# Kernel tuning notes

Hardware: AMD Instinct MI355X
Metric: run time of the kernel (lower is better)

## Reference

```python
import jax, jax.numpy as jnp
import numpy as np

N = 50000
E = 800000
IN_DIM = 128
HIDDEN = 256
HP = HIDDEN // 3            # 85
HP2 = HIDDEN - 2 * HP       # 86
OUT_DIM = 40


def setup_inputs() -> dict:
    key = jax.random.key(0)
    ks = jax.random.split(key, 10)
    x = jax.random.normal(ks[0], (N, IN_DIM), dtype=jnp.float32)
    edge_index = jax.random.randint(ks[1], (2, E), 0, N, dtype=jnp.int64)
    s = 1.0 / np.sqrt(IN_DIM)
    W0 = jax.random.uniform(ks[2], (IN_DIM, HP), jnp.float32, -s, s)
    b0 = jax.random.uniform(ks[3], (HP,), jnp.float32, -s, s)
    W1 = jax.random.uniform(ks[4], (IN_DIM, HP), jnp.float32, -s, s)
    b1 = jax.random.uniform(ks[5], (HP,), jnp.float32, -s, s)
    W2 = jax.random.uniform(ks[6], (IN_DIM, HP2), jnp.float32, -s, s)
    b2 = jax.random.uniform(ks[7], (HP2,), jnp.float32, -s, s)
    sf = 1.0 / np.sqrt(HIDDEN)
    Wf = jax.random.uniform(ks[8], (HIDDEN, OUT_DIM), jnp.float32, -sf, sf)
    bf = jax.random.uniform(ks[9], (OUT_DIM,), jnp.float32, -sf, sf)
    return {"x": x, "edge_index": edge_index, "W0": W0, "b0": b0,
            "W1": W1, "b1": b1, "W2": W2, "b2": b2, "Wf": Wf, "bf": bf}


def _spmm(row, col, x, n):
    # adj @ x where adj[row[e], col[e]] = 1 : gather neighbor feats, scatter-add to row
    return jax.ops.segment_sum(x[col], row, num_segments=n)


def reference(x, edge_index, W0, b0, W1, b1, W2, b2, Wf, bf):
    n = x.shape[0]
    row, col = edge_index[0], edge_index[1]
    # out-degree of row nodes, clamped to min 1
    deg = jax.ops.segment_sum(jnp.ones((row.shape[0],), x.dtype), row, num_segments=n)
    deg_inv = 1.0 / jnp.maximum(deg, 1.0)
    # hop 0
    h0 = x @ W0 + b0
    # hop 1: (A x) * deg_inv
    ax = _spmm(row, col, x, n)
    h1 = (ax * deg_inv[:, None]) @ W1 + b1
    # hop 2: (A A x) * deg_inv^2
    aax = _spmm(row, col, ax, n)
    h2 = (aax * (deg_inv ** 2)[:, None]) @ W2 + b2
    h = jax.nn.relu(jnp.concatenate([h0, h1, h2], axis=1))
    # dropout inactive in eval mode
    return h @ Wf + bf
```

## Files before the change

kernel.cpp:

```cpp
#include <hip/hip_runtime.h>

#define N_NODES 50000
#define E_EDGES 800000
#define IN_DIM  128
#define OUT_DIM 40
#define NPAD    50176
#define NBKT    196
#define NBLK    256
#define EPB     3125

#define OFF_CNT   0
#define OFF_BASE  50176
#define OFF_DEG   100352
#define OFF_RS    150528
#define OFF_EPACK 200704
#define OFF_SCOL  1000704
#define OFF_WTBF  1800704
#define OFF_WF2T  1819136
#define OFF_BV    1826048
#define OFF_XBF   1826336
#define OFF_AXBF  (OFF_XBF  + NPAD * 64)
#define OFF_AAXBF (OFF_AXBF + NPAD * 64)
#define OFF_BTOT  (OFF_AAXBF + NPAD * 64)
#define OFF_BOFF  (OFF_BTOT + 256)

typedef short bf16x8 __attribute__((ext_vector_type(8)));
typedef float f32x4  __attribute__((ext_vector_type(4)));

__device__ __forceinline__ short f2bf(float f) {
    unsigned u = __float_as_uint(f);
    unsigned r = u + 0x7FFFu + ((u >> 16) & 1u);
    return (short)(r >> 16);
}

__device__ __forceinline__ bf16x8 cvt8(float4 a, float4 b) {
    bf16x8 v;
    v[0] = f2bf(a.x); v[1] = f2bf(a.y); v[2] = f2bf(a.z); v[3] = f2bf(a.w);
    v[4] = f2bf(b.x); v[5] = f2bf(b.y); v[6] = f2bf(b.z); v[7] = f2bf(b.w);
    return v;
}

__device__ __forceinline__ int block_excl_scan_256(int v, int* total_out,
                                                   int* wtot )
{
    const int t = threadIdx.x;
    const int lane = t & 63, wid = t >> 6;
    int sc = v;
    #pragma unroll
    for (int off = 1; off < 64; off <<= 1) {
        int tmp = __shfl_up(sc, off, 64);
        if (lane >= off) sc += tmp;
    }
    if (lane == 63) wtot[wid] = sc;
    __syncthreads();
    if (t == 0) {
        int a = 0;
        #pragma unroll
        for (int w2 = 0; w2 < 4; ++w2) { int tmp = wtot[w2]; wtot[w2] = a; a += tmp; }
        wtot[4] = a;
    }
    __syncthreads();
    *total_out = wtot[4];
    return sc - v + wtot[wid];
}

__global__ __launch_bounds__(256) void prep_kernel(
    const float* __restrict__ x, short* __restrict__ xbf,
    const int* __restrict__ row, int* __restrict__ cnt,
    const float* __restrict__ W0, const float* __restrict__ b0,
    const float* __restrict__ W1, const float* __restrict__ b1,
    const float* __restrict__ W2, const float* __restrict__ b2,
    const float* __restrict__ Wf,
    short* __restrict__ Wtbf, short* __restrict__ Wf2t,
    float* __restrict__ biasv)
{
    __shared__ int lbin[NBKT];
    const int t = threadIdx.x;
    const int b = blockIdx.x;

    if (b < 3136) {
        int idx = b * 256 + t;
        int node = idx >> 4;
        bf16x8 v;
        if (node < N_NODES) {
            const float4* rp = (const float4*)x + (size_t)idx * 2;
            v = cvt8(rp[0], rp[1]);
        } else {
            #pragma unroll
            for (int j = 0; j < 8; ++j) v[j] = 0;
        }
        *(bf16x8*)(xbf + (size_t)idx * 8) = v;
    } else if (b < 3136 + NBLK) {
        const int blk = b - 3136;
        if (t < NBKT) lbin[t] = 0;
        __syncthreads();
        const int e0 = blk * EPB;
        for (int i = t; i < EPB; i += 256)
            atomicAdd(&lbin[row[e0 + i] >> 8], 1);
        __syncthreads();
        if (t < NBKT) cnt[t * NBLK + blk] = lbin[t];
    } else {
        int idx = (b - 3392) * 256 + t;
        if (idx < 288 * 128) {
            int v = idx >> 7, k = idx & 127;
            int s = v / 96, local = v - 96 * s;
            float val = 0.0f;
            if (s == 0 && local < 85)      val = W0[k * 85 + local];
            else if (s == 1 && local < 85) val = W1[k * 85 + local];
            else if (s == 2 && local < 86) val = W2[k * 86 + local];
            Wtbf[idx] = f2bf(val);
        } else if (idx < 288 * 128 + 48 * 288) {
            int j2 = idx - 288 * 128;
            int c = j2 / 288, v = j2 - c * 288;
            int s = v / 96, local = v - 96 * s;
            float val = 0.0f;
            if (c < OUT_DIM && local < ((s == 2) ? 86 : 85))
                val = Wf[(s * 85 + local) * OUT_DIM + c];
            Wf2t[j2] = f2bf(val);
        } else if (idx < 288 * 128 + 48 * 288 + 288) {
            int v = idx - (288 * 128 + 48 * 288);
            int s = v / 96, local = v - 96 * s;
            float val = 0.0f;
            if (s == 0 && local < 85)      val = b0[local];
            else if (s == 1 && local < 85) val = b1[local];
            else if (s == 2 && local < 86) val = b2[local];
            biasv[v] = val;
        }
    }
}

__global__ __launch_bounds__(256) void scan_local_kernel(
    const int* __restrict__ cnt, int* __restrict__ base,
    int* __restrict__ btot)
{
    __shared__ int wtot[5];
    const int b = blockIdx.x;
    const int t = threadIdx.x;
    int v = cnt[b * NBLK + t];
    int total;
    int excl = block_excl_scan_256(v, &total, wtot);
    base[b * NBLK + t] = excl;
    if (t == 0) btot[b] = total;
}

__global__ __launch_bounds__(256) void scan_add_kernel(
    const int* __restrict__ btot, int* __restrict__ base)
{
    __shared__ int wtot[5];
    __shared__ int sh[256];
    const int t = threadIdx.x;
    const int b = blockIdx.x;
    int v = (t < NBKT) ? btot[t] : 0;
    int total;
    int excl = block_excl_scan_256(v, &total, wtot);
    sh[t] = excl;
    __syncthreads();
    int off = sh[b];
    base[b * NBLK + t] += off;
}

__global__ __launch_bounds__(256) void scatter_coarse_kernel(
    const int* __restrict__ row, const int* __restrict__ col,
    const int* __restrict__ base, unsigned int* __restrict__ epack)
{
    __shared__ int lcnt[NBKT];
    __shared__ int lbs[NBKT];
    const int t   = threadIdx.x;
    const int blk = blockIdx.x;
    if (t < NBKT) { lcnt[t] = 0; lbs[t] = base[t * NBLK + blk]; }
    __syncthreads();
    const int e0 = blk * EPB;
    for (int i = t; i < EPB; i += 256) {
        int r = row[e0 + i];
        int c = col[e0 + i];
        int cb = r >> 8;
        int loc = atomicAdd(&lcnt[cb], 1);
        epack[lbs[cb] + loc] = ((unsigned)(r & 255) << 16) | (unsigned)c;
    }
}

__global__ __launch_bounds__(256) void fine_sort_kernel(
    const unsigned int* __restrict__ epack,
    const int* __restrict__ base,
    int* __restrict__ sorted_col,
    int* __restrict__ deg, int* __restrict__ row_start)
{
    __shared__ int lhist[1024];
    __shared__ int lbase[1024];
    __shared__ int wtot[5];
    const int t  = threadIdx.x;
    const int cb = blockIdx.x;
    const int s  = base[cb * NBLK];
    const int e2 = (cb == NBKT - 1) ? E_EDGES : base[(cb + 1) * NBLK];

    #pragma unroll
    for (int j = 0; j < 4; ++j) lhist[t * 4 + j] = 0;
    __syncthreads();
    for (int i = s + t; i < e2; i += 256) {
        unsigned p = epack[i];
        int key = (int)((p >> 16) << 2) | (int)((p & 0xFFFFu) >> 14);
        atomicAdd(&lhist[key], 1);
    }
    __syncthreads();

    int h[4];
    int sl = 0;
    #pragma unroll
    for (int j = 0; j < 4; ++j) { h[j] = lhist[t * 4 + j]; sl += h[j]; }
    int total;
    int excl = block_excl_scan_256(sl, &total, wtot);

    int node = cb * 256 + t;
    deg[node]       = sl;
    row_start[node] = s + excl;
    int run = excl;
    #pragma unroll
    for (int j = 0; j < 4; ++j) { lbase[t * 4 + j] = run; run += h[j]; }
    __syncthreads();
    #pragma unroll
    for (int j = 0; j < 4; ++j) lhist[t * 4 + j] = 0;
    __syncthreads();

    for (int i = s + t; i < e2; i += 256) {
        unsigned p = epack[i];
        int col = (int)(p & 0xFFFFu);
        int key = (int)((p >> 16) << 2) | (col >> 14);
        int off = atomicAdd(&lhist[key], 1);
        sorted_col[s + lbase[key] + off] = col;
    }
}

__global__ __launch_bounds__(256) void spmm_gather_kernel(
    const short* __restrict__ src,
    const int*   __restrict__ row_start,
    const int*   __restrict__ sorted_col,
    short*       __restrict__ dst)
{
    int node = (blockIdx.x * 256 + threadIdx.x) >> 4;
    int lane = threadIdx.x & 15;
    if (node >= N_NODES) return;
    int s = row_start[node];
    int e = row_start[node + 1];

    float acc[8];
    #pragma unroll
    for (int j = 0; j < 8; ++j) acc[j] = 0.0f;

    for (int i = s; i < e; i += 8) {
        const int nn = e - i;
        int cidx[8];
        #pragma unroll
        for (int j = 0; j < 8; ++j)
            cidx[j] = sorted_col[i + (j < nn ? j : 0)];
        uint4 v[8];
        #pragma unroll
        for (int j = 0; j < 8; ++j)
            v[j] = *(const uint4*)(src + (size_t)cidx[j] * IN_DIM + lane * 8);
        #pragma unroll
        for (int j = 0; j < 8; ++j) {
            if (j < nn) {
                acc[0] += __uint_as_float(v[j].x << 16);
                acc[1] += __uint_as_float(v[j].x & 0xFFFF0000u);
                acc[2] += __uint_as_float(v[j].y << 16);
                acc[3] += __uint_as_float(v[j].y & 0xFFFF0000u);
                acc[4] += __uint_as_float(v[j].z << 16);
                acc[5] += __uint_as_float(v[j].z & 0xFFFF0000u);
                acc[6] += __uint_as_float(v[j].w << 16);
                acc[7] += __uint_as_float(v[j].w & 0xFFFF0000u);
            }
        }
    }
    bf16x8 r;
    #pragma unroll
    for (int j = 0; j < 8; ++j) r[j] = f2bf(acc[j]);
    *(bf16x8*)(dst + (size_t)node * IN_DIM + lane * 8) = r;
}

#define HTS 296

__global__ __launch_bounds__(256) void dense_fused_kernel(
    const short* __restrict__ xbf,
    const short* __restrict__ axbf,
    const short* __restrict__ aaxbf,
    const int*   __restrict__ deg,
    const short* __restrict__ Wtbf,
    const short* __restrict__ Wf2t,
    const float* __restrict__ biasv,
    const float* __restrict__ bfin,
    float* __restrict__ out)
{
    __shared__ short wbuf[96 * 132];
    __shared__ short htile[64 * HTS];

    const int tid  = threadIdx.x;
    const int w    = tid >> 6;
    const int lane = tid & 63;
    const int il   = lane & 15;
    const int kq   = lane >> 4;
    const int m0   = blockIdx.x * 64 + w * 16;

    float dvj[4];
    #pragma unroll
    for (int j = 0; j < 4; ++j) {
        int node = m0 + kq * 4 + j;
        dvj[j] = 1.0f / fmaxf((float)deg[node], 1.0f);
    }

    #pragma unroll
    for (int s = 0; s < 3; ++s) {
        #pragma unroll
        for (int j = 0; j < 6; ++j) {
            int idx  = tid + j * 256;
            int brow = idx >> 4;
            int slot = idx & 15;
            uint4 v = *(const uint4*)(Wtbf + (size_t)(s * 96 + brow) * IN_DIM + slot * 8);
            *(uint4*)(wbuf + brow * 132 + slot * 8) = v;
        }
        __syncthreads();

        const short* __restrict__ src = (s == 0) ? xbf : (s == 1) ? axbf : aaxbf;
        const int arow = m0 + il;

        f32x4 acc[6];
        #pragma unroll
        for (int c = 0; c < 6; ++c)
            #pragma unroll
            for (int q = 0; q < 4; ++q) acc[c][q] = 0.0f;

        #pragma unroll
        for (int kk = 0; kk < 4; ++kk) {
            bf16x8 afrag = *(const bf16x8*)(
                src + (size_t)arow * IN_DIM + kk * 32 + kq * 8);
            #pragma unroll
            for (int c = 0; c < 6; ++c) {
                bf16x8 bfrag = *(const bf16x8*)(
                    wbuf + (c * 16 + il) * 132 + kk * 32 + kq * 8);
                acc[c] = __builtin_amdgcn_mfma_f32_16x16x32_bf16(
                    afrag, bfrag, acc[c], 0, 0, 0);
            }
        }

        #pragma unroll
        for (int j = 0; j < 4; ++j) {
            int nl = w * 16 + kq * 4 + j;
            float sc = (s == 0) ? 1.0f : (s == 1) ? dvj[j] : dvj[j] * dvj[j];
            #pragma unroll
            for (int c = 0; c < 6; ++c) {
                int vcol = s * 96 + c * 16 + il;
                float hv = fmaf(acc[c][j], sc, biasv[vcol]);
                htile[nl * HTS + vcol] = f2bf(fmaxf(hv, 0.0f));
            }
        }
        __syncthreads();
    }

    f32x4 acc2[3];
    #pragma unroll
    for (int cc = 0; cc < 3; ++cc)
        #pragma unroll
        for (int q = 0; q < 4; ++q) acc2[cc][q] = 0.0f;

    #pragma unroll
    for (int kk = 0; kk < 9; ++kk) {
        bf16x8 afrag = *(const bf16x8*)(
            htile + (w * 16 + il) * HTS + kk * 32 + kq * 8);
        #pragma unroll
        for (int cc = 0; cc < 3; ++cc) {
            bf16x8 bfrag = *(const bf16x8*)(
                Wf2t + (size_t)(cc * 16 + il) * 288 + kk * 32 + kq * 8);
            acc2[cc] = __builtin_amdgcn_mfma_f32_16x16x32_bf16(
                afrag, bfrag, acc2[cc], 0, 0, 0);
        }
    }

    #pragma unroll
    for (int cc = 0; cc < 3; ++cc) {
        int colo = cc * 16 + il;
        if (colo < OUT_DIM) {
            float b = bfin[colo];
            #pragma unroll
            for (int j = 0; j < 4; ++j) {
                int node = m0 + kq * 4 + j;
                if (node < N_NODES)
                    out[(size_t)node * OUT_DIM + colo] = acc2[cc][j] + b;
            }
        }
    }
}

extern "C" void kernel_launch(void* const* d_in, const int* in_sizes, int n_in,
                              void* d_out, int out_size, void* d_ws, size_t ws_size,
                              hipStream_t stream)
{
    const float* x  = (const float*)d_in[0];
    const int*   ei = (const int*)  d_in[1];
    const float* W0 = (const float*)d_in[2];
    const float* b0 = (const float*)d_in[3];
    const float* W1 = (const float*)d_in[4];
    const float* b1 = (const float*)d_in[5];
    const float* W2 = (const float*)d_in[6];
    const float* b2 = (const float*)d_in[7];
    const float* Wf = (const float*)d_in[8];
    const float* bf = (const float*)d_in[9];
    float* out = (float*)d_out;

    const int* row = ei;
    const int* col = ei + E_EDGES;

    int* wsw = (int*)d_ws;
    int*          cnt        = wsw + OFF_CNT;
    int*          base       = wsw + OFF_BASE;
    int*          deg        = wsw + OFF_DEG;
    int*          row_start  = wsw + OFF_RS;
    unsigned int* epack      = (unsigned int*)(wsw + OFF_EPACK);
    int*          sorted_col = wsw + OFF_SCOL;
    short*        Wtbf       = (short*)(wsw + OFF_WTBF);
    short*        Wf2t       = (short*)(wsw + OFF_WF2T);
    float*        biasv      = (float*)(wsw + OFF_BV);
    short*        xbf        = (short*)(wsw + OFF_XBF);
    short*        axbf       = (short*)(wsw + OFF_AXBF);
    short*        aaxbf      = (short*)(wsw + OFF_AAXBF);
    int*          btot       = wsw + OFF_BTOT;
    int*          boff       = wsw + OFF_BOFF;
    (void)boff; (void)ws_size; (void)in_sizes; (void)n_in; (void)out_size;

    dim3 blk(256);
    prep_kernel          <<<3136 + NBLK + 200, blk, 0, stream>>>(
        x, xbf, row, cnt, W0, b0, W1, b1, W2, b2, Wf, Wtbf, Wf2t, biasv);
    scan_local_kernel    <<<NBKT, blk, 0, stream>>>(cnt, base, btot);
    scan_add_kernel      <<<NBKT, blk, 0, stream>>>(btot, base);
    scatter_coarse_kernel<<<NBLK, blk, 0, stream>>>(row, col, base, epack);
    fine_sort_kernel     <<<NBKT, blk, 0, stream>>>(epack, base, sorted_col,
                                                    deg, row_start);

    const int sg = (N_NODES * 16 + 255) / 256;
    spmm_gather_kernel<<<sg, blk, 0, stream>>>(xbf,  row_start, sorted_col, axbf);
    spmm_gather_kernel<<<sg, blk, 0, stream>>>(axbf, row_start, sorted_col, aaxbf);

    dense_fused_kernel<<<NPAD / 64, blk, 0, stream>>>(
        xbf, axbf, aaxbf, deg, Wtbf, Wf2t, biasv, bf, out);
}
```

Baseline: 116.1 us.

## Drop scan_add kernel by recomputing bucket offsets; double-buffer SpMM gathers

Removes the scan_add kernel launch. Each consumer block now recomputes the exclusive scan of the per-bucket totals (btot) itself, in both the scatter and fine-sort kernels, which saves one launch and one global read-modify-write pass over base at the cost of redundant small scans. The SpMM gather loop is restructured to keep two batches of eight neighbor rows in flight, so the loads for the next batch overlap accumulation of the current one. The remainder is handled separately. This raises register pressure and may lower occupancy.

```diff
diff --git a/kernel.cpp b/kernel.cpp
--- a/kernel.cpp
+++ b/kernel.cpp
@@ -143,32 +143,23 @@
     if (t == 0) btot[b] = total;
 }
 
-__global__ __launch_bounds__(256) void scan_add_kernel(
-    const int* __restrict__ btot, int* __restrict__ base)
-{
-    __shared__ int wtot[5];
-    __shared__ int sh[256];
-    const int t = threadIdx.x;
-    const int b = blockIdx.x;
-    int v = (t < NBKT) ? btot[t] : 0;
-    int total;
-    int excl = block_excl_scan_256(v, &total, wtot);
-    sh[t] = excl;
-    __syncthreads();
-    int off = sh[b];
-    base[b * NBLK + t] += off;
-}
-
 __global__ __launch_bounds__(256) void scatter_coarse_kernel(
     const int* __restrict__ row, const int* __restrict__ col,
-    const int* __restrict__ base, unsigned int* __restrict__ epack)
+    const int* __restrict__ base, const int* __restrict__ btot,
+    unsigned int* __restrict__ epack)
 {
     __shared__ int lcnt[NBKT];
     __shared__ int lbs[NBKT];
+    __shared__ int wtot[5];
     const int t   = threadIdx.x;
     const int blk = blockIdx.x;
-    if (t < NBKT) { lcnt[t] = 0; lbs[t] = base[t * NBLK + blk]; }
-    __syncthreads();
+
+    int v = (t < NBKT) ? btot[t] : 0;
+    int tot;
+    int boff = block_excl_scan_256(v, &tot, wtot);
+    if (t < NBKT) { lcnt[t] = 0; lbs[t] = base[t * NBLK + blk] + boff; }
+    __syncthreads();
+
     const int e0 = blk * EPB;
     for (int i = t; i < EPB; i += 256) {
         int r = row[e0 + i];
@@ -181,17 +172,25 @@
 
 __global__ __launch_bounds__(256) void fine_sort_kernel(
     const unsigned int* __restrict__ epack,
-    const int* __restrict__ base,
+    const int* __restrict__ btot,
     int* __restrict__ sorted_col,
     int* __restrict__ deg, int* __restrict__ row_start)
 {
     __shared__ int lhist[1024];
     __shared__ int lbase[1024];
     __shared__ int wtot[5];
+    __shared__ int sb[2];
     const int t  = threadIdx.x;
     const int cb = blockIdx.x;
-    const int s  = base[cb * NBLK];
-    const int e2 = (cb == NBKT - 1) ? E_EDGES : base[(cb + 1) * NBLK];
+
+    int bv = (t < NBKT) ? btot[t] : 0;
+    int btot_sum;
+    int bexcl = block_excl_scan_256(bv, &btot_sum, wtot);
+    if (t == cb)     sb[0] = bexcl;
+    if (t == cb + 1) sb[1] = bexcl;
+    __syncthreads();
+    const int s  = sb[0];
+    const int e2 = sb[1];
 
     #pragma unroll
     for (int j = 0; j < 4; ++j) lhist[t * 4 + j] = 0;
@@ -230,6 +229,22 @@
     }
 }
 
+#define LOADC8(C, base) { _Pragma("unroll") \
+    for (int j = 0; j < 8; ++j) (C)[j] = sorted_col[(base) + j]; }
+#define GATHER8(V, C) { _Pragma("unroll") \
+    for (int j = 0; j < 8; ++j) \
+        (V)[j] = *(const uint4*)(src + (size_t)(C)[j] * IN_DIM + lane * 8); }
+#define CONSUME8(V) { _Pragma("unroll") \
+    for (int j = 0; j < 8; ++j) { \
+        acc[0] += __uint_as_float((V)[j].x << 16); \
+        acc[1] += __uint_as_float((V)[j].x & 0xFFFF0000u); \
+        acc[2] += __uint_as_float((V)[j].y << 16); \
+        acc[3] += __uint_as_float((V)[j].y & 0xFFFF0000u); \
+        acc[4] += __uint_as_float((V)[j].z << 16); \
+        acc[5] += __uint_as_float((V)[j].z & 0xFFFF0000u); \
+        acc[6] += __uint_as_float((V)[j].w << 16); \
+        acc[7] += __uint_as_float((V)[j].w & 0xFFFF0000u); } }
+
 __global__ __launch_bounds__(256) void spmm_gather_kernel(
     const short* __restrict__ src,
     const int*   __restrict__ row_start,
@@ -239,37 +254,54 @@
     int node = (blockIdx.x * 256 + threadIdx.x) >> 4;
     int lane = threadIdx.x & 15;
     if (node >= N_NODES) return;
-    int s = row_start[node];
-    int e = row_start[node + 1];
+    const int s = row_start[node];
+    const int e = row_start[node + 1];
+    const int F = (e - s) >> 3;
 
     float acc[8];
     #pragma unroll
     for (int j = 0; j < 8; ++j) acc[j] = 0.0f;
 
-    for (int i = s; i < e; i += 8) {
-        const int nn = e - i;
-        int cidx[8];
+    int   cA[8], cB[8];
+    uint4 vA[8], vB[8];
+
+    if (F >= 1) { LOADC8(cA, s);     GATHER8(vA, cA); }
+    if (F >= 2) { LOADC8(cB, s + 8); GATHER8(vB, cB); }
+
+    for (int f = 0; f < F; ++f) {
+        if ((f & 1) == 0) {
+            CONSUME8(vA);
+            if (f + 2 < F) { LOADC8(cA, s + (f + 2) * 8); GATHER8(vA, cA); }
+        } else {
+            CONSUME8(vB);
+            if (f + 2 < F) { LOADC8(cB, s + (f + 2) * 8); GATHER8(vB, cB); }
+        }
+    }
+
+    const int it = s + F * 8;
+    const int nn = e - it;
+    if (nn > 0) {
         #pragma unroll
         for (int j = 0; j < 8; ++j)
-            cidx[j] = sorted_col[i + (j < nn ? j : 0)];
-        uint4 v[8];
+            cA[j] = sorted_col[it + (j < nn ? j : 0)];
         #pragma unroll
         for (int j = 0; j < 8; ++j)
-            v[j] = *(const uint4*)(src + (size_t)cidx[j] * IN_DIM + lane * 8);
+            vA[j] = *(const uint4*)(src + (size_t)cA[j] * IN_DIM + lane * 8);
         #pragma unroll
         for (int j = 0; j < 8; ++j) {
             if (j < nn) {
-                acc[0] += __uint_as_float(v[j].x << 16);
-                acc[1] += __uint_as_float(v[j].x & 0xFFFF0000u);
-                acc[2] += __uint_as_float(v[j].y << 16);
-                acc[3] += __uint_as_float(v[j].y & 0xFFFF0000u);
-                acc[4] += __uint_as_float(v[j].z << 16);
-                acc[5] += __uint_as_float(v[j].z & 0xFFFF0000u);
-                acc[6] += __uint_as_float(v[j].w << 16);
-                acc[7] += __uint_as_float(v[j].w & 0xFFFF0000u);
+                acc[0] += __uint_as_float(vA[j].x << 16);
+                acc[1] += __uint_as_float(vA[j].x & 0xFFFF0000u);
+                acc[2] += __uint_as_float(vA[j].y << 16);
+                acc[3] += __uint_as_float(vA[j].y & 0xFFFF0000u);
+                acc[4] += __uint_as_float(vA[j].z << 16);
+                acc[5] += __uint_as_float(vA[j].z & 0xFFFF0000u);
+                acc[6] += __uint_as_float(vA[j].w << 16);
+                acc[7] += __uint_as_float(vA[j].w & 0xFFFF0000u);
             }
         }
     }
+
     bf16x8 r;
     #pragma unroll
     for (int j = 0; j < 8; ++j) r[j] = f2bf(acc[j]);
@@ -421,16 +453,14 @@
     short*        axbf       = (short*)(wsw + OFF_AXBF);
     short*        aaxbf      = (short*)(wsw + OFF_AAXBF);
     int*          btot       = wsw + OFF_BTOT;
-    int*          boff       = wsw + OFF_BOFF;
-    (void)boff; (void)ws_size; (void)in_sizes; (void)n_in; (void)out_size;
+    (void)ws_size; (void)in_sizes; (void)n_in; (void)out_size;
 
     dim3 blk(256);
     prep_kernel          <<<3136 + NBLK + 200, blk, 0, stream>>>(
         x, xbf, row, cnt, W0, b0, W1, b1, W2, b2, Wf, Wtbf, Wf2t, biasv);
     scan_local_kernel    <<<NBKT, blk, 0, stream>>>(cnt, base, btot);
-    scan_add_kernel      <<<NBKT, blk, 0, stream>>>(btot, base);
-    scatter_coarse_kernel<<<NBLK, blk, 0, stream>>>(row, col, base, epack);
-    fine_sort_kernel     <<<NBKT, blk, 0, stream>>>(epack, base, sorted_col,
+    scatter_coarse_kernel<<<NBLK, blk, 0, stream>>>(row, col, base, btot, epack);
+    fine_sort_kernel     <<<NBKT, blk, 0, stream>>>(epack, btot, sorted_col,
                                                     deg, row_start);
 
     const int sg = (N_NODES * 16 + 255) / 256;
```

Result: no change. 116.5 us (+0.4%).
